# Kernel optimization log

Measured on AMD Instinct MI355X. Metric: run time of the kernel, lower is better.

The kernel has to match this reference:

```python
import jax, jax.numpy as jnp
import numpy as np

E = 20000       # num edges (nodes of the edge-adjacency graph)
FDIM = 128      # edge_feature_dim
D = 16          # stalk_dim ('diagonal' => mlp output dim = D)
P = 300000      # number of adjacent (i, j) pairs extracted from L1
EPS = 1e-5      # LayerNorm eps


def _xavier(key, fan_in, fan_out):
    lim = np.sqrt(6.0 / (fan_in + fan_out)).astype(np.float32)
    return jax.random.uniform(key, (fan_in, fan_out), jnp.float32, -lim, lim)


def _layernorm(x, g, b):
    mu = jnp.mean(x, axis=-1, keepdims=True)
    var = jnp.mean((x - mu) ** 2, axis=-1, keepdims=True)
    return (x - mu) * jax.lax.rsqrt(var + EPS) * g + b


def setup_inputs() -> dict:
    key = jax.random.key(0)
    ks = jax.random.split(key, 8)
    return {
        "edge_features": jax.random.normal(ks[0], (E, FDIM), jnp.float32),
        "pair_i": jax.random.randint(ks[1], (P,), 0, E),
        "pair_j": jax.random.randint(ks[2], (P,), 0, E),
        # MLP: Linear(2F,64) -> LN -> ReLU -> Linear(64,32) -> LN -> ReLU -> Linear(32,D)
        "W1": _xavier(ks[3], 2 * FDIM, 64), "b1": jnp.zeros((64,), jnp.float32),
        "g1": jnp.ones((64,), jnp.float32), "be1": jnp.zeros((64,), jnp.float32),
        "W2": _xavier(ks[4], 64, 32), "b2": jnp.zeros((32,), jnp.float32),
        "g2": jnp.ones((32,), jnp.float32), "be2": jnp.zeros((32,), jnp.float32),
        "W3": _xavier(ks[5], 32, D), "b3": jnp.zeros((D,), jnp.float32),
    }


def reference(edge_features, pair_i, pair_j, W1, b1, g1, be1, W2, b2, g2, be2, W3, b3):
    # Gather the two edge feature vectors per adjacent pair and concat: [P, 2F]
    x = jnp.concatenate([edge_features[pair_i], edge_features[pair_j]], axis=1)
    h = jax.nn.relu(_layernorm(x @ W1 + b1, g1, be1))      # [P, 64]
    h = jax.nn.relu(_layernorm(h @ W2 + b2, g2, be2))      # [P, 32]
    params = h @ W3 + b3                                    # [P, D]
    # diagonal sheaf: F_ij = diag(params) for every pair, batched (diag_embed)
    return params[:, :, None] * jnp.eye(D, dtype=params.dtype)  # [P, D, D]
```

## Files before the change

### kernel.cpp

```cpp
#include <hip/hip_runtime.h>
#include <hip/hip_fp16.h>

#if defined(__has_builtin)
#if __has_builtin(__builtin_amdgcn_fdot2)
#define HAVE_FDOT2 1
#endif
#endif

typedef _Float16 hv2 __attribute__((ext_vector_type(2)));

__device__ __forceinline__ float dot2f(__half2 a, __half2 b, float c) {
#ifdef HAVE_FDOT2
    hv2 av = __builtin_bit_cast(hv2, a);
    hv2 bv = __builtin_bit_cast(hv2, b);
    return __builtin_amdgcn_fdot2(av, bv, c, false);
#else
    float2 fa = __half22float2(a), fb = __half22float2(b);
    return fmaf(fa.y, fb.y, fmaf(fa.x, fb.x, c));
#endif
}

__global__ void bad_map_marker(float* out) {
    if (threadIdx.x == 0 && blockIdx.x == 0) out[0] = 1.0e6f;
}

__device__ __forceinline__ void mlp_tail_compute(float* h, float* pr, int D,
        const float* g1, const float* be1,
        const float* W2, const float* b2,
        const float* g2, const float* be2,
        const float* W3, const float* b3) {
    float s = 0.f, ss = 0.f;
    #pragma unroll
    for (int d = 0; d < 64; ++d) { s += h[d]; ss += h[d] * h[d]; }
    float mu  = s * (1.f / 64.f);
    float inv = rsqrtf(ss * (1.f / 64.f) - mu * mu + 1e-5f);
    #pragma unroll
    for (int d = 0; d < 64; ++d)
        h[d] = fmaxf((h[d] - mu) * inv * g1[d] + be1[d], 0.f);

    float a2[32];
    const float4* w2v = (const float4*)W2;
    #pragma unroll
    for (int n = 0; n < 32; ++n) a2[n] = b2[n];
    for (int k = 0; k < 64; ++k) {
        float hk = h[k];
        #pragma unroll
        for (int q = 0; q < 8; ++q) {
            float4 w = w2v[k * 8 + q];
            a2[4 * q + 0] += hk * w.x;
            a2[4 * q + 1] += hk * w.y;
            a2[4 * q + 2] += hk * w.z;
            a2[4 * q + 3] += hk * w.w;
        }
    }
    s = 0.f; ss = 0.f;
    #pragma unroll
    for (int n = 0; n < 32; ++n) { s += a2[n]; ss += a2[n] * a2[n]; }
    mu  = s * (1.f / 32.f);
    inv = rsqrtf(ss * (1.f / 32.f) - mu * mu + 1e-5f);
    #pragma unroll
    for (int n = 0; n < 32; ++n)
        a2[n] = fmaxf((a2[n] - mu) * inv * g2[n] + be2[n], 0.f);

    for (int d = 0; d < D; ++d) pr[d] = b3[d];
    for (int k = 0; k < 32; ++k) {
        float hk = a2[k];
        const float* wr = W3 + k * D;
        for (int d = 0; d < D; ++d) pr[d] += hk * wr[d];
    }
}

__device__ __forceinline__ void store_diag16_f32_256(const float* pp, float* out, int P) {
    const int t = threadIdx.x;
    float4* outv = (float4*)out + (size_t)blockIdx.x * 16384;
    const int pbase = blockIdx.x * 256;
    #pragma unroll 8
    for (int it = 0; it < 64; ++it) {
        int g = it * 256 + t;
        int pl = g >> 6;
        int rem = g & 63;
        int d = rem >> 2;
        int c4 = rem & 3;
        float val = pp[pl * 17 + d];
        bool on = (d >> 2) == c4;
        float4 v;
        v.x = (on && (d & 3) == 0) ? val : 0.f;
        v.y = (on && (d & 3) == 1) ? val : 0.f;
        v.z = (on && (d & 3) == 2) ? val : 0.f;
        v.w = (on && (d & 3) == 3) ? val : 0.f;
        if (pbase + pl < P) outv[g] = v;
    }
}

__global__ __launch_bounds__(256)
void precompute_y(const float* __restrict__ ef, const float* __restrict__ W1,
                  const float* __restrict__ b1, __half* __restrict__ Y, int E) {
    __shared__ __align__(16) float el[64 * 132];
    const int t = threadIdx.x;
    const int ebase = blockIdx.x * 64;

    for (int idx = t; idx < 2048; idx += 256) {
        int er = idx >> 5, ec = idx & 31;
        if (ebase + er < E)
            *((float4*)(el + er * 132) + ec) =
                *((const float4*)(ef + (size_t)(ebase + er) * 128) + ec);
    }
    __syncthreads();

    const int cg = t & 15;
    const int eg = t >> 4;
    const int half_ = cg >> 3;
    const int col64 = (cg & 7) * 8;

    float acc[4][8];
    #pragma unroll
    for (int i = 0; i < 4; ++i)
        #pragma unroll
        for (int c = 0; c < 8; ++c) acc[i][c] = 0.f;

    const float* wbase = W1 + (size_t)half_ * 128 * 64 + col64;
    #pragma unroll 4
    for (int k = 0; k < 128; ++k) {
        float4 w0 = *(const float4*)(wbase + (size_t)k * 64);
        float4 w1 = *(const float4*)(wbase + (size_t)k * 64 + 4);
        float wv[8] = {w0.x, w0.y, w0.z, w0.w, w1.x, w1.y, w1.z, w1.w};
        #pragma unroll
        for (int i = 0; i < 4; ++i) {
            float a = el[(eg * 4 + i) * 132 + k];
            #pragma unroll
            for (int c = 0; c < 8; ++c) acc[i][c] += a * wv[c];
        }
    }

    float bb[8];
    #pragma unroll
    for (int c = 0; c < 8; ++c) bb[c] = (half_ == 0) ? b1[col64 + c] : 0.f;
    #pragma unroll
    for (int i = 0; i < 4; ++i) {
        int e = ebase + eg * 4 + i;
        if (e < E) {
            __half* dst = Y + (size_t)e * 128 + half_ * 64 + col64;
            __half2 hv[4];
            #pragma unroll
            for (int c = 0; c < 4; ++c)
                hv[c] = __floats2half2_rn(acc[i][2 * c] + bb[2 * c],
                                          acc[i][2 * c + 1] + bb[2 * c + 1]);
            *(float4*)dst = *(float4*)hv;
        }
    }
}

__global__ __launch_bounds__(256)
void sheaf_pairs(const int* __restrict__ pi, const int* __restrict__ pj,
                 const __half* __restrict__ Y,
                 const float* __restrict__ g1, const float* __restrict__ be1,
                 const float* __restrict__ W2, const float* __restrict__ b2,
                 const float* __restrict__ g2, const float* __restrict__ be2,
                 const float* __restrict__ W3, const float* __restrict__ b3,
                 float* __restrict__ out, int P) {
    __shared__ float pp[256 * 17];
    __shared__ __align__(16) __half2 w2p[32 * 32];
    __shared__ __align__(16) __half2 w3p[16 * 16];
    __shared__ float g1s[64], be1s[64], b2s[32], g2s[32], be2s[32], b3s[16];

    const int t = threadIdx.x;
    int p = blockIdx.x * 256 + t;
    int pc = p < P ? p : P - 1;
    int i = pi[pc], j = pj[pc];

    const float4* y1 = (const float4*)(Y + (size_t)i * 128);
    const float4* y2 = (const float4*)(Y + (size_t)j * 128 + 64);
    float4 ra[8], rb[8];
    #pragma unroll
    for (int q = 0; q < 8; ++q) { ra[q] = y1[q]; rb[q] = y2[q]; }

    for (int idx = t; idx < 1024; idx += 256) {
        int k2 = idx >> 5, n = idx & 31;
        w2p[k2 * 32 + n] = __floats2half2_rn(W2[(2 * k2) * 32 + n],
                                             W2[(2 * k2 + 1) * 32 + n]);
    }
    if (t < 256) {
        int k2 = t >> 4, n = t & 15;
        w3p[k2 * 16 + n] = __floats2half2_rn(W3[(2 * k2) * 16 + n],
                                             W3[(2 * k2 + 1) * 16 + n]);
    }
    if (t < 64)                 { g1s[t] = g1[t]; be1s[t] = be1[t]; }
    else if (t < 96)            b2s[t - 64]   = b2[t - 64];
    else if (t < 128)           g2s[t - 96]   = g2[t - 96];
    else if (t < 160)           be2s[t - 128] = be2[t - 128];
    else if (t < 176)           b3s[t - 160]  = b3[t - 160];

    float s = 0.f, ss = 0.f;
    #pragma unroll
    for (int q = 0; q < 8; ++q) {
        const __half2* ha = (const __half2*)&ra[q];
        const __half2* hb = (const __half2*)&rb[q];
        #pragma unroll
        for (int u = 0; u < 4; ++u) {
            float2 fa = __half22float2(ha[u]);
            float2 fb = __half22float2(hb[u]);
            float h0 = fa.x + fb.x, h1 = fa.y + fb.y;
            s  += h0 + h1;
            ss += h0 * h0 + h1 * h1;
        }
    }
    float mu  = s * (1.f / 64.f);
    float inv = rsqrtf(ss * (1.f / 64.f) - mu * mu + 1e-5f);

    __syncthreads();

    __half2 hp[32];
    #pragma unroll
    for (int q = 0; q < 8; ++q) {
        const __half2* ha = (const __half2*)&ra[q];
        const __half2* hb = (const __half2*)&rb[q];
        #pragma unroll
        for (int u = 0; u < 4; ++u) {
            int k = 8 * q + 2 * u;
            float2 fa = __half22float2(ha[u]);
            float2 fb = __half22float2(hb[u]);
            float h0 = fmaxf((fa.x + fb.x - mu) * inv * g1s[k]     + be1s[k],     0.f);
            float h1 = fmaxf((fa.y + fb.y - mu) * inv * g1s[k + 1] + be1s[k + 1], 0.f);
            hp[4 * q + u] = __floats2half2_rn(h0, h1);
        }
    }

    float a2[32];
    #pragma unroll
    for (int n = 0; n < 32; ++n) a2[n] = b2s[n];
    #pragma unroll 8
    for (int k2 = 0; k2 < 32; ++k2) {
        __half2 hk = hp[k2];
        const float4* wrow = (const float4*)(w2p + k2 * 32);
        #pragma unroll
        for (int u = 0; u < 8; ++u) {
            float4 wq = wrow[u];
            const __half2* wp = (const __half2*)&wq;
            a2[4 * u + 0] = dot2f(hk, wp[0], a2[4 * u + 0]);
            a2[4 * u + 1] = dot2f(hk, wp[1], a2[4 * u + 1]);
            a2[4 * u + 2] = dot2f(hk, wp[2], a2[4 * u + 2]);
            a2[4 * u + 3] = dot2f(hk, wp[3], a2[4 * u + 3]);
        }
    }

    s = 0.f; ss = 0.f;
    #pragma unroll
    for (int n = 0; n < 32; ++n) { s += a2[n]; ss += a2[n] * a2[n]; }
    mu  = s * (1.f / 32.f);
    inv = rsqrtf(ss * (1.f / 32.f) - mu * mu + 1e-5f);
    #pragma unroll
    for (int n = 0; n < 32; ++n)
        a2[n] = fmaxf((a2[n] - mu) * inv * g2s[n] + be2s[n], 0.f);

    __half2 ap[16];
    #pragma unroll
    for (int k2 = 0; k2 < 16; ++k2) ap[k2] = __floats2half2_rn(a2[2 * k2], a2[2 * k2 + 1]);

    float pr[16];
    #pragma unroll
    for (int d = 0; d < 16; ++d) pr[d] = b3s[d];
    #pragma unroll 4
    for (int k2 = 0; k2 < 16; ++k2) {
        __half2 ak = ap[k2];
        const float4* wrow = (const float4*)(w3p + k2 * 16);
        #pragma unroll
        for (int u = 0; u < 4; ++u) {
            float4 wq = wrow[u];
            const __half2* wp = (const __half2*)&wq;
            pr[4 * u + 0] = dot2f(ak, wp[0], pr[4 * u + 0]);
            pr[4 * u + 1] = dot2f(ak, wp[1], pr[4 * u + 1]);
            pr[4 * u + 2] = dot2f(ak, wp[2], pr[4 * u + 2]);
            pr[4 * u + 3] = dot2f(ak, wp[3], pr[4 * u + 3]);
        }
    }

    #pragma unroll
    for (int d = 0; d < 16; ++d) pp[t * 17 + d] = pr[d];
    __syncthreads();
    store_diag16_f32_256(pp, out, P);
}

__global__ __launch_bounds__(256)
void sheaf_generic(const float* __restrict__ ef,
                   const int* __restrict__ pi, const int* __restrict__ pj,
                   const float* __restrict__ W1, const float* __restrict__ b1,
                   const float* __restrict__ g1, const float* __restrict__ be1,
                   const float* __restrict__ W2, const float* __restrict__ b2,
                   const float* __restrict__ g2, const float* __restrict__ be2,
                   const float* __restrict__ W3, const float* __restrict__ b3,
                   float* __restrict__ out, int P, int F, int D) {
    __shared__ float pp[256 * 17];
    int p = blockIdx.x * 256 + threadIdx.x;
    int pc = p < P ? p : P - 1;
    int i = pi[pc], j = pj[pc];
    const float* efi = ef + (size_t)i * F;
    const float* efj = ef + (size_t)j * F;
    float h[64];
    #pragma unroll
    for (int n = 0; n < 64; ++n) h[n] = b1[n];
    for (int k = 0; k < F; ++k) {
        float ei = efi[k];
        float ej = efj[k];
        const float* wi = W1 + (size_t)k * 64;
        const float* wj = W1 + (size_t)(F + k) * 64;
        #pragma unroll
        for (int n = 0; n < 64; ++n) h[n] += ei * wi[n] + ej * wj[n];
    }
    float pr[32];
    mlp_tail_compute(h, pr, D, g1, be1, W2, b2, g2, be2, W3, b3);

    if (D == 16) {
        #pragma unroll
        for (int d = 0; d < 16; ++d) pp[threadIdx.x * 17 + d] = pr[d];
        __syncthreads();
        store_diag16_f32_256(pp, out, P);
    } else {
        if (p < P) {
            float* po = out + (size_t)p * D * D;
            for (int r = 0; r < D; ++r) {
                float dv = pr[r];
                for (int c = 0; c < D; ++c) po[r * D + c] = (r == c) ? dv : 0.f;
            }
        }
    }
}

struct Map { int ef, pi, pj, w1, b1, g1, be1, w2, b2, g2, be2, w3, b3; };

static bool validate_map(const Map& m, const int* s, int n_in, long out_size,
                         int* Fo, int* Eo, int* Do, int* Po) {
    if (n_in < 13) return false;
    if (s[m.b1] != 64 || s[m.g1] != 64 || s[m.be1] != 64) return false;
    if (s[m.b2] != 32 || s[m.g2] != 32 || s[m.be2] != 32) return false;
    if (s[m.w2] != 64 * 32) return false;
    long w1 = s[m.w1];
    if (w1 <= 0 || (w1 % 128) != 0) return false;
    long F = w1 / 128;
    if (F <= 0) return false;
    int D = s[m.b3];
    if (D <= 0 || D > 32) return false;
    if (s[m.w3] != 32 * D) return false;
    long P = s[m.pi];
    if (P <= 0 || s[m.pj] != P) return false;
    long ef = s[m.ef];
    if (ef <= 0 || (ef % F) != 0) return false;
    long E = ef / F;
    if (out_size != P * D * D) return false;
    *Fo = (int)F; *Eo = (int)E; *Do = D; *Po = (int)P;
    return true;
}

extern "C" void kernel_launch(void* const* d_in, const int* in_sizes, int n_in,
                              void* d_out, int out_size, void* d_ws, size_t ws_size,
                              hipStream_t stream) {
    const Map pos   = {0, 1, 2, 3, 4, 5, 6, 7, 8, 9, 10, 11, 12};
    const Map alpha = {8, 11, 12, 0, 3, 9, 6, 1, 4, 10, 7, 2, 5};

    int F = 0, E = 0, D = 0, P = 0;
    Map m;
    if (validate_map(pos, in_sizes, n_in, (long)out_size, &F, &E, &D, &P)) {
        m = pos;
    } else if (validate_map(alpha, in_sizes, n_in, (long)out_size, &F, &E, &D, &P)) {
        m = alpha;
    } else {
        bad_map_marker<<<dim3(1), dim3(64), 0, stream>>>((float*)d_out);
        return;
    }

    const float* ef  = (const float*)d_in[m.ef];
    const int*   pi  = (const int*)d_in[m.pi];
    const int*   pj  = (const int*)d_in[m.pj];
    const float* W1  = (const float*)d_in[m.w1];
    const float* b1  = (const float*)d_in[m.b1];
    const float* g1  = (const float*)d_in[m.g1];
    const float* be1 = (const float*)d_in[m.be1];
    const float* W2  = (const float*)d_in[m.w2];
    const float* b2  = (const float*)d_in[m.b2];
    const float* g2  = (const float*)d_in[m.g2];
    const float* be2 = (const float*)d_in[m.be2];
    const float* W3  = (const float*)d_in[m.w3];
    const float* b3  = (const float*)d_in[m.b3];
    float* out = (float*)d_out;

    const size_t y_bytes = (size_t)E * 128 * sizeof(__half);

    if (F == 128 && D == 16 && ws_size >= y_bytes) {
        __half* Y = (__half*)d_ws;
        precompute_y<<<dim3((E + 63) / 64), dim3(256), 0, stream>>>(ef, W1, b1, Y, E);
        sheaf_pairs<<<dim3((P + 255) / 256), dim3(256), 0, stream>>>(
            pi, pj, Y, g1, be1, W2, b2, g2, be2, W3, b3, out, P);
    } else {
        sheaf_generic<<<dim3((P + 255) / 256), dim3(256), 0, stream>>>(
            ef, pi, pj, W1, b1, g1, be1, W2, b2, g2, be2, W3, b3, out, P, F, D);
    }
}
```

Measured before the change: 389.3 us.

## Make sheaf_pairs persistent with software-pipelined prefetch of next tile gathers

After: 393.0 us. No clear change (+1.0%).

```diff
diff --git a/kernel.cpp b/kernel.cpp
--- a/kernel.cpp
+++ b/kernel.cpp
@@ -70,10 +70,11 @@
     }
 }
 
-__device__ __forceinline__ void store_diag16_f32_256(const float* pp, float* out, int P) {
+__device__ __forceinline__ void store_diag16_tile(const float* pp, float* out,
+                                                  int P, int tile) {
     const int t = threadIdx.x;
-    float4* outv = (float4*)out + (size_t)blockIdx.x * 16384;
-    const int pbase = blockIdx.x * 256;
+    float4* outv = (float4*)out + (size_t)tile * 16384;
+    const int pbase = tile * 256;
     #pragma unroll 8
     for (int it = 0; it < 64; ++it) {
         int g = it * 256 + t;
@@ -150,6 +151,24 @@
     }
 }
 
+__device__ __forceinline__ void load_idx(const int* __restrict__ pi,
+                                         const int* __restrict__ pj,
+                                         int tile, int ntiles, int t, int P,
+                                         int& ii, int& jj) {
+    int tl = tile < ntiles - 1 ? tile : ntiles - 1;
+    int p  = tl * 256 + t;
+    int pc = p < P ? p : P - 1;
+    ii = pi[pc]; jj = pj[pc];
+}
+
+__device__ __forceinline__ void gather_y(const __half* __restrict__ Y,
+                                         int i, int j, float4* ra, float4* rb) {
+    const float4* y1 = (const float4*)(Y + (size_t)i * 128);
+    const float4* y2 = (const float4*)(Y + (size_t)j * 128 + 64);
+    #pragma unroll
+    for (int q = 0; q < 8; ++q) { ra[q] = y1[q]; rb[q] = y2[q]; }
+}
+
 __global__ __launch_bounds__(256)
 void sheaf_pairs(const int* __restrict__ pi, const int* __restrict__ pj,
                  const __half* __restrict__ Y,
@@ -157,29 +176,21 @@
                  const float* __restrict__ W2, const float* __restrict__ b2,
                  const float* __restrict__ g2, const float* __restrict__ be2,
                  const float* __restrict__ W3, const float* __restrict__ b3,
-                 float* __restrict__ out, int P) {
+                 float* __restrict__ out, int P, int ntiles) {
     __shared__ float pp[256 * 17];
     __shared__ __align__(16) __half2 w2p[32 * 32];
     __shared__ __align__(16) __half2 w3p[16 * 16];
     __shared__ float g1s[64], be1s[64], b2s[32], g2s[32], be2s[32], b3s[16];
 
     const int t = threadIdx.x;
-    int p = blockIdx.x * 256 + t;
-    int pc = p < P ? p : P - 1;
-    int i = pi[pc], j = pj[pc];
-
-    const float4* y1 = (const float4*)(Y + (size_t)i * 128);
-    const float4* y2 = (const float4*)(Y + (size_t)j * 128 + 64);
-    float4 ra[8], rb[8];
-    #pragma unroll
-    for (int q = 0; q < 8; ++q) { ra[q] = y1[q]; rb[q] = y2[q]; }
+    const int G = gridDim.x;
 
     for (int idx = t; idx < 1024; idx += 256) {
         int k2 = idx >> 5, n = idx & 31;
         w2p[k2 * 32 + n] = __floats2half2_rn(W2[(2 * k2) * 32 + n],
                                              W2[(2 * k2 + 1) * 32 + n]);
     }
-    if (t < 256) {
+    {
         int k2 = t >> 4, n = t & 15;
         w3p[k2 * 16 + n] = __floats2half2_rn(W3[(2 * k2) * 16 + n],
                                              W3[(2 * k2 + 1) * 16 + n]);
@@ -190,94 +201,118 @@
     else if (t < 160)           be2s[t - 128] = be2[t - 128];
     else if (t < 176)           b3s[t - 160]  = b3[t - 160];
 
-    float s = 0.f, ss = 0.f;
-    #pragma unroll
-    for (int q = 0; q < 8; ++q) {
-        const __half2* ha = (const __half2*)&ra[q];
-        const __half2* hb = (const __half2*)&rb[q];
-        #pragma unroll
-        for (int u = 0; u < 4; ++u) {
-            float2 fa = __half22float2(ha[u]);
-            float2 fb = __half22float2(hb[u]);
-            float h0 = fa.x + fb.x, h1 = fa.y + fb.y;
-            s  += h0 + h1;
-            ss += h0 * h0 + h1 * h1;
-        }
-    }
-    float mu  = s * (1.f / 64.f);
-    float inv = rsqrtf(ss * (1.f / 64.f) - mu * mu + 1e-5f);
+    int tile = blockIdx.x;
+    int tn   = tile + G;
+    int ic, jc, in_, jn_;
+    load_idx(pi, pj, tile, ntiles, t, P, ic, jc);
+    float4 ra[8], rb[8];
+    gather_y(Y, ic, jc, ra, rb);
+    load_idx(pi, pj, tn, ntiles, t, P, in_, jn_);
 
     __syncthreads();
 
-    __half2 hp[32];
-    #pragma unroll
-    for (int q = 0; q < 8; ++q) {
-        const __half2* ha = (const __half2*)&ra[q];
-        const __half2* hb = (const __half2*)&rb[q];
-        #pragma unroll
-        for (int u = 0; u < 4; ++u) {
-            int k = 8 * q + 2 * u;
-            float2 fa = __half22float2(ha[u]);
-            float2 fb = __half22float2(hb[u]);
-            float h0 = fmaxf((fa.x + fb.x - mu) * inv * g1s[k]     + be1s[k],     0.f);
-            float h1 = fmaxf((fa.y + fb.y - mu) * inv * g1s[k + 1] + be1s[k + 1], 0.f);
-            hp[4 * q + u] = __floats2half2_rn(h0, h1);
-        }
-    }
-
-    float a2[32];
-    #pragma unroll
-    for (int n = 0; n < 32; ++n) a2[n] = b2s[n];
-    #pragma unroll 8
-    for (int k2 = 0; k2 < 32; ++k2) {
-        __half2 hk = hp[k2];
-        const float4* wrow = (const float4*)(w2p + k2 * 32);
-        #pragma unroll
-        for (int u = 0; u < 8; ++u) {
-            float4 wq = wrow[u];
-            const __half2* wp = (const __half2*)&wq;
-            a2[4 * u + 0] = dot2f(hk, wp[0], a2[4 * u + 0]);
-            a2[4 * u + 1] = dot2f(hk, wp[1], a2[4 * u + 1]);
-            a2[4 * u + 2] = dot2f(hk, wp[2], a2[4 * u + 2]);
-            a2[4 * u + 3] = dot2f(hk, wp[3], a2[4 * u + 3]);
-        }
-    }
-
-    s = 0.f; ss = 0.f;
-    #pragma unroll
-    for (int n = 0; n < 32; ++n) { s += a2[n]; ss += a2[n] * a2[n]; }
-    mu  = s * (1.f / 32.f);
-    inv = rsqrtf(ss * (1.f / 32.f) - mu * mu + 1e-5f);
-    #pragma unroll
-    for (int n = 0; n < 32; ++n)
-        a2[n] = fmaxf((a2[n] - mu) * inv * g2s[n] + be2s[n], 0.f);
-
-    __half2 ap[16];
-    #pragma unroll
-    for (int k2 = 0; k2 < 16; ++k2) ap[k2] = __floats2half2_rn(a2[2 * k2], a2[2 * k2 + 1]);
-
-    float pr[16];
-    #pragma unroll
-    for (int d = 0; d < 16; ++d) pr[d] = b3s[d];
-    #pragma unroll 4
-    for (int k2 = 0; k2 < 16; ++k2) {
-        __half2 ak = ap[k2];
-        const float4* wrow = (const float4*)(w3p + k2 * 16);
-        #pragma unroll
-        for (int u = 0; u < 4; ++u) {
-            float4 wq = wrow[u];
-            const __half2* wp = (const __half2*)&wq;
-            pr[4 * u + 0] = dot2f(ak, wp[0], pr[4 * u + 0]);
-            pr[4 * u + 1] = dot2f(ak, wp[1], pr[4 * u + 1]);
-            pr[4 * u + 2] = dot2f(ak, wp[2], pr[4 * u + 2]);
-            pr[4 * u + 3] = dot2f(ak, wp[3], pr[4 * u + 3]);
-        }
-    }
-
-    #pragma unroll
-    for (int d = 0; d < 16; ++d) pp[t * 17 + d] = pr[d];
-    __syncthreads();
-    store_diag16_f32_256(pp, out, P);
+    for (;;) {
+        float s = 0.f, ss = 0.f;
+        #pragma unroll
+        for (int q = 0; q < 8; ++q) {
+            const __half2* ha = (const __half2*)&ra[q];
+            const __half2* hb = (const __half2*)&rb[q];
+            #pragma unroll
+            for (int u = 0; u < 4; ++u) {
+                float2 fa = __half22float2(ha[u]);
+                float2 fb = __half22float2(hb[u]);
+                float h0 = fa.x + fb.x, h1 = fa.y + fb.y;
+                s  += h0 + h1;
+                ss += h0 * h0 + h1 * h1;
+            }
+        }
+        float mu  = s * (1.f / 64.f);
+        float inv = rsqrtf(ss * (1.f / 64.f) - mu * mu + 1e-5f);
+
+        __half2 hp[32];
+        #pragma unroll
+        for (int q = 0; q < 8; ++q) {
+            const __half2* ha = (const __half2*)&ra[q];
+            const __half2* hb = (const __half2*)&rb[q];
+            #pragma unroll
+            for (int u = 0; u < 4; ++u) {
+                int k = 8 * q + 2 * u;
+                float2 fa = __half22float2(ha[u]);
+                float2 fb = __half22float2(hb[u]);
+                float h0 = fmaxf((fa.x + fb.x - mu) * inv * g1s[k]     + be1s[k],     0.f);
+                float h1 = fmaxf((fa.y + fb.y - mu) * inv * g1s[k + 1] + be1s[k + 1], 0.f);
+                hp[4 * q + u] = __floats2half2_rn(h0, h1);
+            }
+        }
+
+        float4 na[8], nb[8];
+        gather_y(Y, in_, jn_, na, nb);
+        int tnn = tn + G;
+        int in2, jn2;
+        load_idx(pi, pj, tnn, ntiles, t, P, in2, jn2);
+
+        float a2[32];
+        #pragma unroll
+        for (int n = 0; n < 32; ++n) a2[n] = b2s[n];
+        #pragma unroll 8
+        for (int k2 = 0; k2 < 32; ++k2) {
+            __half2 hk = hp[k2];
+            const float4* wrow = (const float4*)(w2p + k2 * 32);
+            #pragma unroll
+            for (int u = 0; u < 8; ++u) {
+                float4 wq = wrow[u];
+                const __half2* wp = (const __half2*)&wq;
+                a2[4 * u + 0] = dot2f(hk, wp[0], a2[4 * u + 0]);
+                a2[4 * u + 1] = dot2f(hk, wp[1], a2[4 * u + 1]);
+                a2[4 * u + 2] = dot2f(hk, wp[2], a2[4 * u + 2]);
+                a2[4 * u + 3] = dot2f(hk, wp[3], a2[4 * u + 3]);
+            }
+        }
+
+        s = 0.f; ss = 0.f;
+        #pragma unroll
+        for (int n = 0; n < 32; ++n) { s += a2[n]; ss += a2[n] * a2[n]; }
+        mu  = s * (1.f / 32.f);
+        inv = rsqrtf(ss * (1.f / 32.f) - mu * mu + 1e-5f);
+        #pragma unroll
+        for (int n = 0; n < 32; ++n)
+            a2[n] = fmaxf((a2[n] - mu) * inv * g2s[n] + be2s[n], 0.f);
+
+        __half2 ap[16];
+        #pragma unroll
+        for (int k2 = 0; k2 < 16; ++k2)
+            ap[k2] = __floats2half2_rn(a2[2 * k2], a2[2 * k2 + 1]);
+
+        float pr[16];
+        #pragma unroll
+        for (int d = 0; d < 16; ++d) pr[d] = b3s[d];
+        #pragma unroll 4
+        for (int k2 = 0; k2 < 16; ++k2) {
+            __half2 ak = ap[k2];
+            const float4* wrow = (const float4*)(w3p + k2 * 16);
+            #pragma unroll
+            for (int u = 0; u < 4; ++u) {
+                float4 wq = wrow[u];
+                const __half2* wp = (const __half2*)&wq;
+                pr[4 * u + 0] = dot2f(ak, wp[0], pr[4 * u + 0]);
+                pr[4 * u + 1] = dot2f(ak, wp[1], pr[4 * u + 1]);
+                pr[4 * u + 2] = dot2f(ak, wp[2], pr[4 * u + 2]);
+                pr[4 * u + 3] = dot2f(ak, wp[3], pr[4 * u + 3]);
+            }
+        }
+
+        #pragma unroll
+        for (int d = 0; d < 16; ++d) pp[t * 17 + d] = pr[d];
+        __syncthreads();
+        store_diag16_tile(pp, out, P, tile);
+        __syncthreads();
+
+        if (tn >= ntiles) break;
+        #pragma unroll
+        for (int q = 0; q < 8; ++q) { ra[q] = na[q]; rb[q] = nb[q]; }
+        in_ = in2; jn_ = jn2;
+        tile = tn; tn = tnn;
+    }
 }
 
 __global__ __launch_bounds__(256)
@@ -313,7 +348,7 @@
         #pragma unroll
         for (int d = 0; d < 16; ++d) pp[threadIdx.x * 17 + d] = pr[d];
         __syncthreads();
-        store_diag16_f32_256(pp, out, P);
+        store_diag16_tile(pp, out, P, blockIdx.x);
     } else {
         if (p < P) {
             float* po = out + (size_t)p * D * D;
@@ -387,8 +422,10 @@
     if (F == 128 && D == 16 && ws_size >= y_bytes) {
         __half* Y = (__half*)d_ws;
         precompute_y<<<dim3((E + 63) / 64), dim3(256), 0, stream>>>(ef, W1, b1, Y, E);
-        sheaf_pairs<<<dim3((P + 255) / 256), dim3(256), 0, stream>>>(
-            pi, pj, Y, g1, be1, W2, b2, g2, be2, W3, b3, out, P);
+        int ntiles = (P + 255) / 256;
+        int G = ntiles < 512 ? ntiles : 512;
+        sheaf_pairs<<<dim3(G), dim3(256), 0, stream>>>(
+            pi, pj, Y, g1, be1, W2, b2, g2, be2, W3, b3, out, P, ntiles);
     } else {
         sheaf_generic<<<dim3((P + 255) / 256), dim3(256), 0, stream>>>(
             ef, pi, pj, W1, b1, g1, be1, W2, b2, g2, be2, W3, b3, out, P, F, D);
```

## Split each pair across four threads with shuffle reductions in sheaf kernel

Applied to the files above, without the earlier changes.

Result: slower. 401.5 us (+3.1%).

```diff
diff --git a/kernel.cpp b/kernel.cpp
--- a/kernel.cpp
+++ b/kernel.cpp
@@ -70,10 +70,11 @@
     }
 }
 
-__device__ __forceinline__ void store_diag16_f32_256(const float* pp, float* out, int P) {
+__device__ __forceinline__ void store_diag16_tile256(const float* pp, float* out,
+                                                     int P, int tile) {
     const int t = threadIdx.x;
-    float4* outv = (float4*)out + (size_t)blockIdx.x * 16384;
-    const int pbase = blockIdx.x * 256;
+    float4* outv = (float4*)out + (size_t)tile * 16384;
+    const int pbase = tile * 256;
     #pragma unroll 8
     for (int it = 0; it < 64; ++it) {
         int g = it * 256 + t;
@@ -150,102 +151,131 @@
     }
 }
 
-__global__ __launch_bounds__(256)
-void sheaf_pairs(const int* __restrict__ pi, const int* __restrict__ pj,
-                 const __half* __restrict__ Y,
-                 const float* __restrict__ g1, const float* __restrict__ be1,
-                 const float* __restrict__ W2, const float* __restrict__ b2,
-                 const float* __restrict__ g2, const float* __restrict__ be2,
-                 const float* __restrict__ W3, const float* __restrict__ b3,
-                 float* __restrict__ out, int P) {
-    __shared__ float pp[256 * 17];
-    __shared__ __align__(16) __half2 w2p[32 * 32];
+__global__ __launch_bounds__(1024)
+void sheaf_pairs_quad(const int* __restrict__ pi, const int* __restrict__ pj,
+                      const __half* __restrict__ Y,
+                      const float* __restrict__ g1, const float* __restrict__ be1,
+                      const float* __restrict__ W2, const float* __restrict__ b2,
+                      const float* __restrict__ g2, const float* __restrict__ be2,
+                      const float* __restrict__ W3, const float* __restrict__ b3,
+                      float* __restrict__ out, int P) {
+    __shared__ float pp[256 * 20];
+    __shared__ __align__(16) __half2 w2p[32 * 36];
     __shared__ __align__(16) __half2 w3p[16 * 16];
     __shared__ float g1s[64], be1s[64], b2s[32], g2s[32], be2s[32], b3s[16];
 
-    const int t = threadIdx.x;
-    int p = blockIdx.x * 256 + t;
+    const int t  = threadIdx.x;
+    const int pl = t >> 2;
+    const int q  = t & 3;
+    const int pbase = blockIdx.x * 256;
+    int p  = pbase + pl;
     int pc = p < P ? p : P - 1;
     int i = pi[pc], j = pj[pc];
 
-    const float4* y1 = (const float4*)(Y + (size_t)i * 128);
-    const float4* y2 = (const float4*)(Y + (size_t)j * 128 + 64);
-    float4 ra[8], rb[8];
-    #pragma unroll
-    for (int q = 0; q < 8; ++q) { ra[q] = y1[q]; rb[q] = y2[q]; }
-
-    for (int idx = t; idx < 1024; idx += 256) {
-        int k2 = idx >> 5, n = idx & 31;
-        w2p[k2 * 32 + n] = __floats2half2_rn(W2[(2 * k2) * 32 + n],
+    const char* rowi = (const char*)(Y + (size_t)i * 128);
+    const char* rowj = (const char*)(Y + (size_t)j * 128);
+    float4 a0 = *(const float4*)(rowi + q * 16);
+    float4 a1 = *(const float4*)(rowi + 64 + q * 16);
+    float4 b0 = *(const float4*)(rowj + 128 + q * 16);
+    float4 b1 = *(const float4*)(rowj + 192 + q * 16);
+
+    {
+        int k2 = t >> 5, n = t & 31;
+        w2p[k2 * 36 + n] = __floats2half2_rn(W2[(2 * k2) * 32 + n],
                                              W2[(2 * k2 + 1) * 32 + n]);
-    }
-    if (t < 256) {
-        int k2 = t >> 4, n = t & 15;
-        w3p[k2 * 16 + n] = __floats2half2_rn(W3[(2 * k2) * 16 + n],
-                                             W3[(2 * k2 + 1) * 16 + n]);
-    }
-    if (t < 64)                 { g1s[t] = g1[t]; be1s[t] = be1[t]; }
-    else if (t < 96)            b2s[t - 64]   = b2[t - 64];
-    else if (t < 128)           g2s[t - 96]   = g2[t - 96];
-    else if (t < 160)           be2s[t - 128] = be2[t - 128];
-    else if (t < 176)           b3s[t - 160]  = b3[t - 160];
+        if (t < 256) {
+            int k2b = t >> 4, nb = t & 15;
+            w3p[k2b * 16 + nb] = __floats2half2_rn(W3[(2 * k2b) * 16 + nb],
+                                                   W3[(2 * k2b + 1) * 16 + nb]);
+        }
+        if (t < 64)                 { g1s[t] = g1[t]; be1s[t] = be1[t]; }
+        else if (t < 96)            b2s[t - 64]   = b2[t - 64];
+        else if (t < 128)           g2s[t - 96]   = g2[t - 96];
+        else if (t < 160)           be2s[t - 128] = be2[t - 128];
+        else if (t < 176)           b3s[t - 160]  = b3[t - 160];
+    }
+
+    float h[16];
+    {
+        const __half2* pa = (const __half2*)&a0;
+        const __half2* pb = (const __half2*)&b0;
+        #pragma unroll
+        for (int u = 0; u < 4; ++u) {
+            float2 fa = __half22float2(pa[u]);
+            float2 fb = __half22float2(pb[u]);
+            h[2 * u + 0] = fa.x + fb.x;
+            h[2 * u + 1] = fa.y + fb.y;
+        }
+        const __half2* pa1 = (const __half2*)&a1;
+        const __half2* pb1 = (const __half2*)&b1;
+        #pragma unroll
+        for (int u = 0; u < 4; ++u) {
+            float2 fa = __half22float2(pa1[u]);
+            float2 fb = __half22float2(pb1[u]);
+            h[8 + 2 * u + 0] = fa.x + fb.x;
+            h[8 + 2 * u + 1] = fa.y + fb.y;
+        }
+    }
 
     float s = 0.f, ss = 0.f;
     #pragma unroll
-    for (int q = 0; q < 8; ++q) {
-        const __half2* ha = (const __half2*)&ra[q];
-        const __half2* hb = (const __half2*)&rb[q];
-        #pragma unroll
-        for (int u = 0; u < 4; ++u) {
-            float2 fa = __half22float2(ha[u]);
-            float2 fb = __half22float2(hb[u]);
-            float h0 = fa.x + fb.x, h1 = fa.y + fb.y;
-            s  += h0 + h1;
-            ss += h0 * h0 + h1 * h1;
-        }
-    }
+    for (int m = 0; m < 16; ++m) { s += h[m]; ss += h[m] * h[m]; }
+    s  += __shfl_xor(s, 1);  ss += __shfl_xor(ss, 1);
+    s  += __shfl_xor(s, 2);  ss += __shfl_xor(ss, 2);
     float mu  = s * (1.f / 64.f);
     float inv = rsqrtf(ss * (1.f / 64.f) - mu * mu + 1e-5f);
 
     __syncthreads();
 
-    __half2 hp[32];
-    #pragma unroll
-    for (int q = 0; q < 8; ++q) {
-        const __half2* ha = (const __half2*)&ra[q];
-        const __half2* hb = (const __half2*)&rb[q];
-        #pragma unroll
-        for (int u = 0; u < 4; ++u) {
-            int k = 8 * q + 2 * u;
-            float2 fa = __half22float2(ha[u]);
-            float2 fb = __half22float2(hb[u]);
-            float h0 = fmaxf((fa.x + fb.x - mu) * inv * g1s[k]     + be1s[k],     0.f);
-            float h1 = fmaxf((fa.y + fb.y - mu) * inv * g1s[k + 1] + be1s[k + 1], 0.f);
-            hp[4 * q + u] = __floats2half2_rn(h0, h1);
-        }
+    __half2 hp[8];
+    #pragma unroll
+    for (int m2 = 0; m2 < 4; ++m2) {
+        int k = 8 * q + 2 * m2;
+        float h0 = fmaxf((h[2 * m2]     - mu) * inv * g1s[k]     + be1s[k],     0.f);
+        float h1 = fmaxf((h[2 * m2 + 1] - mu) * inv * g1s[k + 1] + be1s[k + 1], 0.f);
+        hp[m2] = __floats2half2_rn(h0, h1);
+    }
+    #pragma unroll
+    for (int m2 = 0; m2 < 4; ++m2) {
+        int k = 32 + 8 * q + 2 * m2;
+        float h0 = fmaxf((h[8 + 2 * m2]     - mu) * inv * g1s[k]     + be1s[k],     0.f);
+        float h1 = fmaxf((h[8 + 2 * m2 + 1] - mu) * inv * g1s[k + 1] + be1s[k + 1], 0.f);
+        hp[4 + m2] = __floats2half2_rn(h0, h1);
     }
 
     float a2[32];
     #pragma unroll
-    for (int n = 0; n < 32; ++n) a2[n] = b2s[n];
-    #pragma unroll 8
-    for (int k2 = 0; k2 < 32; ++k2) {
-        __half2 hk = hp[k2];
-        const float4* wrow = (const float4*)(w2p + k2 * 32);
-        #pragma unroll
-        for (int u = 0; u < 8; ++u) {
-            float4 wq = wrow[u];
-            const __half2* wp = (const __half2*)&wq;
-            a2[4 * u + 0] = dot2f(hk, wp[0], a2[4 * u + 0]);
-            a2[4 * u + 1] = dot2f(hk, wp[1], a2[4 * u + 1]);
-            a2[4 * u + 2] = dot2f(hk, wp[2], a2[4 * u + 2]);
-            a2[4 * u + 3] = dot2f(hk, wp[3], a2[4 * u + 3]);
-        }
+    for (int n = 0; n < 32; ++n) a2[n] = 0.f;
+    #pragma unroll
+    for (int d = 0; d < 4; ++d) {
+        #pragma unroll
+        for (int g = 0; g < 2; ++g) {
+            int k2 = (g == 0) ? (4 * q + d) : (16 + 4 * q + d);
+            __half2 hk = hp[4 * g + d];
+            const float4* wrow = (const float4*)(w2p + k2 * 36);
+            #pragma unroll
+            for (int u = 0; u < 8; ++u) {
+                float4 wq = wrow[u];
+                const __half2* wp = (const __half2*)&wq;
+                a2[4 * u + 0] = dot2f(hk, wp[0], a2[4 * u + 0]);
+                a2[4 * u + 1] = dot2f(hk, wp[1], a2[4 * u + 1]);
+                a2[4 * u + 2] = dot2f(hk, wp[2], a2[4 * u + 2]);
+                a2[4 * u + 3] = dot2f(hk, wp[3], a2[4 * u + 3]);
+            }
+        }
+    }
+    #pragma unroll
+    for (int n = 0; n < 32; ++n) {
+        a2[n] += __shfl_xor(a2[n], 1);
+        a2[n] += __shfl_xor(a2[n], 2);
     }
 
     s = 0.f; ss = 0.f;
     #pragma unroll
-    for (int n = 0; n < 32; ++n) { s += a2[n]; ss += a2[n] * a2[n]; }
+    for (int n = 0; n < 32; ++n) {
+        a2[n] += b2s[n];
+        s += a2[n]; ss += a2[n] * a2[n];
+    }
     mu  = s * (1.f / 32.f);
     inv = rsqrtf(ss * (1.f / 32.f) - mu * mu + 1e-5f);
     #pragma unroll
@@ -254,30 +284,41 @@
 
     __half2 ap[16];
     #pragma unroll
-    for (int k2 = 0; k2 < 16; ++k2) ap[k2] = __floats2half2_rn(a2[2 * k2], a2[2 * k2 + 1]);
-
-    float pr[16];
-    #pragma unroll
-    for (int d = 0; d < 16; ++d) pr[d] = b3s[d];
+    for (int k2 = 0; k2 < 16; ++k2)
+        ap[k2] = __floats2half2_rn(a2[2 * k2], a2[2 * k2 + 1]);
+
+    float pr0 = b3s[4 * q + 0], pr1 = b3s[4 * q + 1];
+    float pr2 = b3s[4 * q + 2], pr3 = b3s[4 * q + 3];
     #pragma unroll 4
     for (int k2 = 0; k2 < 16; ++k2) {
+        float4 wq = *(const float4*)(w3p + k2 * 16 + 4 * q);
+        const __half2* wp = (const __half2*)&wq;
         __half2 ak = ap[k2];
-        const float4* wrow = (const float4*)(w3p + k2 * 16);
-        #pragma unroll
-        for (int u = 0; u < 4; ++u) {
-            float4 wq = wrow[u];
-            const __half2* wp = (const __half2*)&wq;
-            pr[4 * u + 0] = dot2f(ak, wp[0], pr[4 * u + 0]);
-            pr[4 * u + 1] = dot2f(ak, wp[1], pr[4 * u + 1]);
-            pr[4 * u + 2] = dot2f(ak, wp[2], pr[4 * u + 2]);
-            pr[4 * u + 3] = dot2f(ak, wp[3], pr[4 * u + 3]);
-        }
-    }
-
-    #pragma unroll
-    for (int d = 0; d < 16; ++d) pp[t * 17 + d] = pr[d];
+        pr0 = dot2f(ak, wp[0], pr0);
+        pr1 = dot2f(ak, wp[1], pr1);
+        pr2 = dot2f(ak, wp[2], pr2);
+        pr3 = dot2f(ak, wp[3], pr3);
+    }
+    *(float4*)(pp + pl * 20 + 4 * q) = make_float4(pr0, pr1, pr2, pr3);
     __syncthreads();
-    store_diag16_f32_256(pp, out, P);
+
+    float4* outv = (float4*)out + (size_t)blockIdx.x * 16384;
+    #pragma unroll 4
+    for (int it = 0; it < 16; ++it) {
+        int g = it * 1024 + t;
+        int pl2 = g >> 6;
+        int rem = g & 63;
+        int d = rem >> 2;
+        int c4 = rem & 3;
+        float val = pp[pl2 * 20 + d];
+        bool on = (d >> 2) == c4;
+        float4 v;
+        v.x = (on && (d & 3) == 0) ? val : 0.f;
+        v.y = (on && (d & 3) == 1) ? val : 0.f;
+        v.z = (on && (d & 3) == 2) ? val : 0.f;
+        v.w = (on && (d & 3) == 3) ? val : 0.f;
+        if (pbase + pl2 < P) outv[g] = v;
+    }
 }
 
 __global__ __launch_bounds__(256)
@@ -313,7 +354,7 @@
         #pragma unroll
         for (int d = 0; d < 16; ++d) pp[threadIdx.x * 17 + d] = pr[d];
         __syncthreads();
-        store_diag16_f32_256(pp, out, P);
+        store_diag16_tile256(pp, out, P, blockIdx.x);
     } else {
         if (p < P) {
             float* po = out + (size_t)p * D * D;
@@ -387,7 +428,8 @@
     if (F == 128 && D == 16 && ws_size >= y_bytes) {
         __half* Y = (__half*)d_ws;
         precompute_y<<<dim3((E + 63) / 64), dim3(256), 0, stream>>>(ef, W1, b1, Y, E);
-        sheaf_pairs<<<dim3((P + 255) / 256), dim3(256), 0, stream>>>(
+        int ntiles = (P + 255) / 256;
+        sheaf_pairs_quad<<<dim3(ntiles), dim3(1024), 0, stream>>>(
             pi, pj, Y, g1, be1, W2, b2, g2, be2, W3, b3, out, P);
     } else {
         sheaf_generic<<<dim3((P + 255) / 256), dim3(256), 0, stream>>>(
```
